# Optimization experiments

Measured on AMD Instinct MI355X. Metric: run time of the kernel, lower is better.

Reference implementation:

```python
import jax, jax.numpy as jnp
import numpy as np

N_NODES = 100000
N_EDGES = 3200000
D_IN = 128
D_OUT = 128


def setup_inputs() -> dict:
    key = jax.random.key(0)
    ks = jax.random.split(key, 7)
    x = jax.random.normal(ks[0], (N_NODES, D_IN), dtype=jnp.float32)
    weight = jax.random.normal(ks[1], (D_IN, D_OUT), dtype=jnp.float32) * (1.0 / np.sqrt(D_OUT))
    bias = jax.random.normal(ks[2], (D_OUT,), dtype=jnp.float32) * (1.0 / np.sqrt(D_OUT))
    adj_rows = jax.random.randint(ks[3], (N_EDGES,), 0, N_NODES, dtype=jnp.int32)
    adj_cols = jax.random.randint(ks[4], (N_EDGES,), 0, N_NODES, dtype=jnp.int32)
    adj_vals = jax.random.uniform(ks[5], (N_EDGES,), dtype=jnp.float32)
    # norm kept in [0.5, 1.5) to avoid division blow-up (degree-like normalizer)
    norm = jax.random.uniform(ks[6], (N_NODES, 1), dtype=jnp.float32) + 0.5
    return {"x": x, "weight": weight, "bias": bias,
            "adj_rows": adj_rows, "adj_cols": adj_cols, "adj_vals": adj_vals,
            "norm": norm}


def reference(x, weight, bias, adj_rows, adj_cols, adj_vals, norm):
    # support = input @ W               [N, D_OUT]
    support = x @ weight
    # output = spmm(adj, support): gather source rows, scale by edge value,
    # scatter-add into destination rows.
    gathered = support[adj_cols] * adj_vals[:, None]          # [E, D_OUT]
    output = jax.ops.segment_sum(gathered, adj_rows, num_segments=x.shape[0])
    output = output / norm
    return output + bias
```

## Files before the change

### kernel.cpp

```cpp
#include <hip/hip_runtime.h>

#define M_NODES 100000
#define N_EDGES 3200000
#define D 128
#define NBUCK 1563
#define FILL_CHUNK 12288
#define FILL_BLOCKS 261
#define GEMM_BLOCKS 782
#define PREP_BLOCKS (FILL_BLOCKS + GEMM_BLOCKS)
#define BUCK_CAP 4096

#define OFF_SUP16  0ull
#define OFF_BCNT   25600000ull
#define OFF_REC    25608192ull
#define WS_NEEDED  76824576ull

__device__ __forceinline__ unsigned short f2bf(float f) {
    unsigned u = __float_as_uint(f);
    u += 0x7fff + ((u >> 16) & 1);
    return (unsigned short)(u >> 16);
}
__device__ __forceinline__ float2 bfpair(unsigned u) {
    float2 r;
    r.x = __uint_as_float(u << 16);
    r.y = __uint_as_float(u & 0xffff0000u);
    return r;
}

__global__ __launch_bounds__(512) void prep_kernel(const float* __restrict__ x,
                                                   const float* __restrict__ w,
                                                   unsigned* __restrict__ sup16,
                                                   const int* __restrict__ rows,
                                                   const int* __restrict__ cols,
                                                   const float* __restrict__ vals,
                                                   int* __restrict__ bcnt,
                                                   int2* __restrict__ rec,
                                                   int M) {
    __shared__ __align__(16) char smem[37120];
    const int tid = threadIdx.x;

    if (blockIdx.x < FILL_BLOCKS) {
        int* cnt = (int*)smem;
        int* bas = (int*)(smem + 6256);
        unsigned short* lrank = (unsigned short*)(smem + 12512);
        for (int i = tid; i < NBUCK; i += 512) cnt[i] = 0;
        __syncthreads();
        const long long base = (long long)blockIdx.x * FILL_CHUNK;

#pragma unroll
        for (int i = 0; i < 6; ++i) {
            const int li = (i * 512 + tid) * 4;
            const long long e = base + li;
            if (e < N_EDGES) {
                const int4 r = *(const int4*)&rows[e];
                lrank[li + 0] = (unsigned short)atomicAdd(&cnt[r.x >> 6], 1);
                lrank[li + 1] = (unsigned short)atomicAdd(&cnt[r.y >> 6], 1);
                lrank[li + 2] = (unsigned short)atomicAdd(&cnt[r.z >> 6], 1);
                lrank[li + 3] = (unsigned short)atomicAdd(&cnt[r.w >> 6], 1);
            }
        }
        __syncthreads();
        for (int i = tid; i < NBUCK; i += 512)
            bas[i] = cnt[i] ? atomicAdd(&bcnt[i], cnt[i]) : 0;
        __syncthreads();
#pragma unroll
        for (int i = 0; i < 6; ++i) {
            const int li = (i * 512 + tid) * 4;
            const long long e = base + li;
            if (e < N_EDGES) {
                const int4   r = *(const int4*)&rows[e];
                const int4   c = *(const int4*)&cols[e];
                const float4 v = *(const float4*)&vals[e];
                int p;
                p = bas[r.x >> 6] + lrank[li + 0];
                if (p < BUCK_CAP)
                    rec[(size_t)(r.x >> 6) * BUCK_CAP + p] =
                        make_int2(c.x | ((r.x & 63) << 20), __float_as_int(v.x));
                p = bas[r.y >> 6] + lrank[li + 1];
                if (p < BUCK_CAP)
                    rec[(size_t)(r.y >> 6) * BUCK_CAP + p] =
                        make_int2(c.y | ((r.y & 63) << 20), __float_as_int(v.y));
                p = bas[r.z >> 6] + lrank[li + 2];
                if (p < BUCK_CAP)
                    rec[(size_t)(r.z >> 6) * BUCK_CAP + p] =
                        make_int2(c.z | ((r.z & 63) << 20), __float_as_int(v.z));
                p = bas[r.w >> 6] + lrank[li + 3];
                if (p < BUCK_CAP)
                    rec[(size_t)(r.w >> 6) * BUCK_CAP + p] =
                        make_int2(c.w | ((r.w & 63) << 20), __float_as_int(v.w));
            }
        }
        return;
    }

    float (*sX)[128] = (float(*)[128])smem;
    float (*sW)[128] = (float(*)[128])(smem + 16384);

    const int r0 = (blockIdx.x - FILL_BLOCKS) * 128;
    const int tx = tid & 31;
    const int ty = tid >> 5;

    float acc[8][4];
#pragma unroll
    for (int r = 0; r < 8; ++r)
#pragma unroll
        for (int c = 0; c < 4; ++c) acc[r][c] = 0.f;

    for (int c0 = 0; c0 < 128; c0 += 32) {
        {
            const int row = tid >> 3;
            const int kk  = (tid & 7) * 4;
#pragma unroll
            for (int h = 0; h < 2; ++h) {
                const int rr = row + h * 64;
                float4 v = make_float4(0.f, 0.f, 0.f, 0.f);
                if (r0 + rr < M)
                    v = *(const float4*)&x[(size_t)(r0 + rr) * D + c0 + kk];
                sX[kk + 0][rr] = v.x;
                sX[kk + 1][rr] = v.y;
                sX[kk + 2][rr] = v.z;
                sX[kk + 3][rr] = v.w;
            }
        }
#pragma unroll
        for (int i = tid; i < 1024; i += 512) {
            const int k  = i >> 5;
            const int c4 = (i & 31) * 4;
            *(float4*)&sW[k][c4] = *(const float4*)&w[(size_t)(c0 + k) * D + c4];
        }
        __syncthreads();

#pragma unroll
        for (int k = 0; k < 32; ++k) {
            const float4 wv = *(const float4*)&sW[k][tx * 4];
            const float4 xa = *(const float4*)&sX[k][ty * 8];
            const float4 xb = *(const float4*)&sX[k][ty * 8 + 4];
            const float xr[8] = {xa.x, xa.y, xa.z, xa.w, xb.x, xb.y, xb.z, xb.w};
#pragma unroll
            for (int r = 0; r < 8; ++r) {
                acc[r][0] += xr[r] * wv.x;
                acc[r][1] += xr[r] * wv.y;
                acc[r][2] += xr[r] * wv.z;
                acc[r][3] += xr[r] * wv.w;
            }
        }
        __syncthreads();
    }

#pragma unroll
    for (int r = 0; r < 8; ++r) {
        const int row = r0 + ty * 8 + r;
        if (row < M) {
            uint2 p;
            p.x = (unsigned)f2bf(acc[r][0]) | ((unsigned)f2bf(acc[r][1]) << 16);
            p.y = (unsigned)f2bf(acc[r][2]) | ((unsigned)f2bf(acc[r][3]) << 16);
            *(uint2*)&sup16[(size_t)row * 64 + tx * 2] = p;
        }
    }
}

__global__ __launch_bounds__(512) void gather_kernel(const unsigned* __restrict__ sup16,
                                                     const int* __restrict__ bcnt,
                                                     const int2* __restrict__ rec,
                                                     const float* __restrict__ norm,
                                                     const float* __restrict__ bias,
                                                     float* __restrict__ out) {
    __shared__ int2 elist[BUCK_CAP];
    __shared__ int cnt[64];
    __shared__ int rbase[65];
    const int tid = threadIdx.x;
    const int b   = blockIdx.x;

    if (tid < 64) cnt[tid] = 0;
    __syncthreads();
    const int n = min(bcnt[b], BUCK_CAP);
    const int2* __restrict__ recb = rec + (size_t)b * BUCK_CAP;

    for (int k = tid; k < n; k += 512)
        atomicAdd(&cnt[(recb[k].x >> 20) & 63], 1);
    __syncthreads();
    if (tid == 0) {
        int run = 0;
#pragma unroll
        for (int i = 0; i < 64; ++i) {
            rbase[i] = run;
            run += cnt[i];
        }
        rbase[64] = run;
    }
    __syncthreads();
    if (tid < 64) cnt[tid] = rbase[tid];
    __syncthreads();
    for (int k = tid; k < n; k += 512) {
        const int2 e = recb[k];
        const int p = atomicAdd(&cnt[(e.x >> 20) & 63], 1);
        elist[p] = make_int2(e.x & 0xFFFFF, e.y);
    }
    __syncthreads();

    const int w    = tid >> 6;
    const int lane = tid & 63;
    const unsigned* __restrict__ supl = sup16 + lane;
    const int fo = lane * 2;
    const float2 b2 = *(const float2*)&bias[fo];

#pragma unroll 1
    for (int rr = 0; rr < 8; ++rr) {
        const int rl  = w * 8 + rr;
        const int row = b * 64 + rl;
        if (row >= M_NODES) break;
        const int j0 = rbase[rl];
        const int j1 = rbase[rl + 1];
        float2 acc = make_float2(0.f, 0.f);
        int j = j0;
        for (; j + 8 <= j1; j += 8) {
            int2 e[8];
#pragma unroll
            for (int q = 0; q < 8; ++q) e[q] = elist[j + q];
            unsigned u[8];
#pragma unroll
            for (int q = 0; q < 8; ++q) u[q] = supl[(unsigned)e[q].x << 6];
#pragma unroll
            for (int q = 0; q < 8; ++q) {
                const float v = __int_as_float(e[q].y);
                const float2 p = bfpair(u[q]);
                acc.x = fmaf(p.x, v, acc.x);
                acc.y = fmaf(p.y, v, acc.y);
            }
        }
        for (; j + 2 <= j1; j += 2) {
            const int2 e0 = elist[j];
            const int2 e1 = elist[j + 1];
            const unsigned u0 = supl[(unsigned)e0.x << 6];
            const unsigned u1 = supl[(unsigned)e1.x << 6];
            const float2 p0 = bfpair(u0);
            const float2 p1 = bfpair(u1);
            const float v0 = __int_as_float(e0.y);
            const float v1 = __int_as_float(e1.y);
            acc.x = fmaf(p0.x, v0, acc.x);
            acc.y = fmaf(p0.y, v0, acc.y);
            acc.x = fmaf(p1.x, v1, acc.x);
            acc.y = fmaf(p1.y, v1, acc.y);
        }
        for (; j < j1; ++j) {
            const int2 e = elist[j];
            const unsigned u = supl[(unsigned)e.x << 6];
            const float v = __int_as_float(e.y);
            const float2 p = bfpair(u);
            acc.x = fmaf(p.x, v, acc.x);
            acc.y = fmaf(p.y, v, acc.y);
        }
        const float inv = 1.0f / norm[row];
        float2 o;
        o.x = fmaf(acc.x, inv, b2.x);
        o.y = fmaf(acc.y, inv, b2.y);
        *(float2*)&out[(size_t)row * D + fo] = o;
    }
}

__global__ __launch_bounds__(256) void gemm32_kernel(const float* __restrict__ x,
                                                     const float* __restrict__ w,
                                                     float* __restrict__ support,
                                                     int M) {
    __shared__ float sX[32][64];
    __shared__ float sW[32][128];
    const int tid = threadIdx.x;
    const int r0  = blockIdx.x * 64;
    const int tx  = tid & 31;
    const int ty  = tid >> 5;
    float acc[8][4];
#pragma unroll
    for (int r = 0; r < 8; ++r)
#pragma unroll
        for (int c = 0; c < 4; ++c) acc[r][c] = 0.f;
    for (int c0 = 0; c0 < 128; c0 += 32) {
        {
            const int row = tid >> 3;
            const int kk  = (tid & 7) * 4;
#pragma unroll
            for (int h = 0; h < 2; ++h) {
                const int rr = row + h * 32;
                float4 v = make_float4(0.f, 0.f, 0.f, 0.f);
                if (r0 + rr < M)
                    v = *(const float4*)&x[(size_t)(r0 + rr) * D + c0 + kk];
                sX[kk + 0][rr] = v.x; sX[kk + 1][rr] = v.y;
                sX[kk + 2][rr] = v.z; sX[kk + 3][rr] = v.w;
            }
        }
#pragma unroll
        for (int i = tid; i < 1024; i += 256) {
            const int k  = i >> 5;
            const int c4 = (i & 31) * 4;
            *(float4*)&sW[k][c4] = *(const float4*)&w[(size_t)(c0 + k) * D + c4];
        }
        __syncthreads();
#pragma unroll
        for (int k = 0; k < 32; ++k) {
            const float4 wv = *(const float4*)&sW[k][tx * 4];
            const float4 xa = *(const float4*)&sX[k][ty * 8];
            const float4 xb = *(const float4*)&sX[k][ty * 8 + 4];
            const float xr[8] = {xa.x, xa.y, xa.z, xa.w, xb.x, xb.y, xb.z, xb.w};
#pragma unroll
            for (int r = 0; r < 8; ++r) {
                acc[r][0] += xr[r] * wv.x; acc[r][1] += xr[r] * wv.y;
                acc[r][2] += xr[r] * wv.z; acc[r][3] += xr[r] * wv.w;
            }
        }
        __syncthreads();
    }
#pragma unroll
    for (int r = 0; r < 8; ++r) {
        const int row = r0 + ty * 8 + r;
        if (row < M)
            *(float4*)&support[(size_t)row * D + tx * 4] =
                make_float4(acc[r][0], acc[r][1], acc[r][2], acc[r][3]);
    }
}

__global__ __launch_bounds__(256) void spmm_kernel(const float* __restrict__ support,
                                                   const int* __restrict__ rows,
                                                   const int* __restrict__ cols,
                                                   const float* __restrict__ vals,
                                                   float* __restrict__ out) {
    const long long t = (long long)blockIdx.x * 256 + threadIdx.x;
    const int e = (int)(t >> 5);
    if (e >= N_EDGES) return;
    const int f   = (int)(t & 31) * 4;
    const int src = cols[e];
    const int dst = rows[e];
    const float v = vals[e];
    const float4 s = *(const float4*)&support[(size_t)src * D + f];
    float* o = &out[(size_t)dst * D + f];
    atomicAdd(o + 0, s.x * v);
    atomicAdd(o + 1, s.y * v);
    atomicAdd(o + 2, s.z * v);
    atomicAdd(o + 3, s.w * v);
}

__global__ __launch_bounds__(256) void finalize_kernel(float* __restrict__ out,
                                                       const float* __restrict__ norm,
                                                       const float* __restrict__ bias) {
    const int t = blockIdx.x * 256 + threadIdx.x;
    const int nrow = t >> 5;
    if (nrow >= M_NODES) return;
    const int f = (t & 31) * 4;
    const float inv = 1.0f / norm[nrow];
    float4 o = *(float4*)&out[(size_t)nrow * D + f];
    const float4 b = *(const float4*)&bias[f];
    o.x = o.x * inv + b.x; o.y = o.y * inv + b.y;
    o.z = o.z * inv + b.z; o.w = o.w * inv + b.w;
    *(float4*)&out[(size_t)nrow * D + f] = o;
}

extern "C" void kernel_launch(void* const* d_in, const int* in_sizes, int n_in,
                              void* d_out, int out_size, void* d_ws, size_t ws_size,
                              hipStream_t stream) {
    const float* x    = (const float*)d_in[0];
    const float* w    = (const float*)d_in[1];
    const float* bias = (const float*)d_in[2];
    const int*   rows = (const int*)d_in[3];
    const int*   cols = (const int*)d_in[4];
    const float* vals = (const float*)d_in[5];
    const float* norm = (const float*)d_in[6];
    float* out = (float*)d_out;
    char* ws = (char*)d_ws;

    if (ws_size >= WS_NEEDED) {
        unsigned* sup16 = (unsigned*)(ws + OFF_SUP16);
        int*      bcnt  = (int*)(ws + OFF_BCNT);
        int2*     rec   = (int2*)(ws + OFF_REC);

        hipMemsetAsync(bcnt, 0, NBUCK * sizeof(int), stream);
        prep_kernel<<<PREP_BLOCKS, 512, 0, stream>>>(x, w, sup16, rows, cols, vals,
                                                     bcnt, rec, M_NODES);
        gather_kernel<<<NBUCK, 512, 0, stream>>>(sup16, bcnt, rec,
                                                 norm, bias, out);
    } else {
        float* support = (float*)ws;
        gemm32_kernel<<<(M_NODES + 63) / 64, 256, 0, stream>>>(x, w, support, M_NODES);
        hipMemsetAsync(d_out, 0, (size_t)out_size * sizeof(float), stream);
        const long long spmm_threads = (long long)N_EDGES * 32;
        spmm_kernel<<<(int)((spmm_threads + 255) / 256), 256, 0, stream>>>(support, rows, cols, vals, out);
        finalize_kernel<<<(M_NODES * 32 + 255) / 256, 256, 0, stream>>>(out, norm, bias);
    }
}
```

Measured before the change: 331.3 us.

## Sort bucket edges by source-node segment to improve gather locality

The gather kernel now bins each bucket's edges by (source-node segment of 16K nodes, destination row) rather than by destination row alone, using a 512-entry block-wide prefix scan in place of the serial 64-entry scan. Each wave then walks the seven source segments in order, keeping eight row accumulators in registers. At any moment all blocks are then reading support rows from a narrower address range, which should improve L2/MALL hit rate on the random gathers. In exchange it adds scan barriers, more registers, and shorter inner loops (unroll 4 instead of 8) with more loop overhead per segment.

```diff
diff --git a/kernel.cpp b/kernel.cpp
--- a/kernel.cpp
+++ b/kernel.cpp
@@ -9,6 +9,7 @@
 #define GEMM_BLOCKS 782
 #define PREP_BLOCKS (FILL_BLOCKS + GEMM_BLOCKS)
 #define BUCK_CAP 4096
+#define NSEG 7
 
 #define OFF_SUP16  0ull
 #define OFF_BCNT   25600000ull
@@ -166,34 +167,41 @@
                                                      const float* __restrict__ bias,
                                                      float* __restrict__ out) {
     __shared__ int2 elist[BUCK_CAP];
-    __shared__ int cnt[64];
-    __shared__ int rbase[65];
+    __shared__ int cnt[512];
+    __shared__ int rbase[514];
     const int tid = threadIdx.x;
     const int b   = blockIdx.x;
 
-    if (tid < 64) cnt[tid] = 0;
+    cnt[tid] = 0;
     __syncthreads();
     const int n = min(bcnt[b], BUCK_CAP);
     const int2* __restrict__ recb = rec + (size_t)b * BUCK_CAP;
 
-    for (int k = tid; k < n; k += 512)
-        atomicAdd(&cnt[(recb[k].x >> 20) & 63], 1);
-    __syncthreads();
-    if (tid == 0) {
-        int run = 0;
-#pragma unroll
-        for (int i = 0; i < 64; ++i) {
-            rbase[i] = run;
-            run += cnt[i];
-        }
-        rbase[64] = run;
-    }
-    __syncthreads();
-    if (tid < 64) cnt[tid] = rbase[tid];
+    for (int k = tid; k < n; k += 512) {
+        const int ex = recb[k].x;
+        const int key = (((ex & 0xFFFFF) >> 14) << 6) | ((ex >> 20) & 63);
+        atomicAdd(&cnt[key], 1);
+    }
+    __syncthreads();
+    int* tsum = (int*)elist;
+    const int myc = cnt[tid];
+    tsum[tid] = myc;
+    __syncthreads();
+    for (int off = 1; off < 512; off <<= 1) {
+        const int v = (tid >= off) ? tsum[tid - off] : 0;
+        __syncthreads();
+        tsum[tid] += v;
+        __syncthreads();
+    }
+    const int excl = tsum[tid] - myc;
+    rbase[tid] = excl;
+    cnt[tid]   = excl;
+    if (tid == 0) rbase[512] = n;
     __syncthreads();
     for (int k = tid; k < n; k += 512) {
         const int2 e = recb[k];
-        const int p = atomicAdd(&cnt[(e.x >> 20) & 63], 1);
+        const int key = (((e.x & 0xFFFFF) >> 14) << 6) | ((e.x >> 20) & 63);
+        const int p = atomicAdd(&cnt[key], 1);
         elist[p] = make_int2(e.x & 0xFFFFF, e.y);
     }
     __syncthreads();
@@ -204,57 +212,55 @@
     const int fo = lane * 2;
     const float2 b2 = *(const float2*)&bias[fo];
 
+    float2 acc[8];
+#pragma unroll
+    for (int r = 0; r < 8; ++r) acc[r] = make_float2(0.f, 0.f);
+
 #pragma unroll 1
+    for (int seg = 0; seg < NSEG; ++seg) {
+        const int kbase = seg * 64 + w * 8;
+#pragma unroll
+        for (int rr = 0; rr < 8; ++rr) {
+            int j = rbase[kbase + rr];
+            const int j1 = rbase[kbase + rr + 1];
+            float2 a = acc[rr];
+            for (; j + 4 <= j1; j += 4) {
+                int2 e[4];
+#pragma unroll
+                for (int q = 0; q < 4; ++q) e[q] = elist[j + q];
+                unsigned u[4];
+#pragma unroll
+                for (int q = 0; q < 4; ++q) u[q] = supl[(unsigned)e[q].x << 6];
+#pragma unroll
+                for (int q = 0; q < 4; ++q) {
+                    const float v = __int_as_float(e[q].y);
+                    const float2 p = bfpair(u[q]);
+                    a.x = fmaf(p.x, v, a.x);
+                    a.y = fmaf(p.y, v, a.y);
+                }
+            }
+            for (; j < j1; ++j) {
+                const int2 e = elist[j];
+                const unsigned u = supl[(unsigned)e.x << 6];
+                const float v = __int_as_float(e.y);
+                const float2 p = bfpair(u);
+                a.x = fmaf(p.x, v, a.x);
+                a.y = fmaf(p.y, v, a.y);
+            }
+            acc[rr] = a;
+        }
+    }
+
+#pragma unroll
     for (int rr = 0; rr < 8; ++rr) {
-        const int rl  = w * 8 + rr;
-        const int row = b * 64 + rl;
-        if (row >= M_NODES) break;
-        const int j0 = rbase[rl];
-        const int j1 = rbase[rl + 1];
-        float2 acc = make_float2(0.f, 0.f);
-        int j = j0;
-        for (; j + 8 <= j1; j += 8) {
-            int2 e[8];
-#pragma unroll
-            for (int q = 0; q < 8; ++q) e[q] = elist[j + q];
-            unsigned u[8];
-#pragma unroll
-            for (int q = 0; q < 8; ++q) u[q] = supl[(unsigned)e[q].x << 6];
-#pragma unroll
-            for (int q = 0; q < 8; ++q) {
-                const float v = __int_as_float(e[q].y);
-                const float2 p = bfpair(u[q]);
-                acc.x = fmaf(p.x, v, acc.x);
-                acc.y = fmaf(p.y, v, acc.y);
-            }
-        }
-        for (; j + 2 <= j1; j += 2) {
-            const int2 e0 = elist[j];
-            const int2 e1 = elist[j + 1];
-            const unsigned u0 = supl[(unsigned)e0.x << 6];
-            const unsigned u1 = supl[(unsigned)e1.x << 6];
-            const float2 p0 = bfpair(u0);
-            const float2 p1 = bfpair(u1);
-            const float v0 = __int_as_float(e0.y);
-            const float v1 = __int_as_float(e1.y);
-            acc.x = fmaf(p0.x, v0, acc.x);
-            acc.y = fmaf(p0.y, v0, acc.y);
-            acc.x = fmaf(p1.x, v1, acc.x);
-            acc.y = fmaf(p1.y, v1, acc.y);
-        }
-        for (; j < j1; ++j) {
-            const int2 e = elist[j];
-            const unsigned u = supl[(unsigned)e.x << 6];
-            const float v = __int_as_float(e.y);
-            const float2 p = bfpair(u);
-            acc.x = fmaf(p.x, v, acc.x);
-            acc.y = fmaf(p.y, v, acc.y);
-        }
-        const float inv = 1.0f / norm[row];
-        float2 o;
-        o.x = fmaf(acc.x, inv, b2.x);
-        o.y = fmaf(acc.y, inv, b2.y);
-        *(float2*)&out[(size_t)row * D + fo] = o;
+        const int row = b * 64 + w * 8 + rr;
+        if (row < M_NODES) {
+            const float inv = 1.0f / norm[row];
+            float2 o;
+            o.x = fmaf(acc[rr].x, inv, b2.x);
+            o.y = fmaf(acc[rr].y, inv, b2.y);
+            *(float2*)&out[(size_t)row * D + fo] = o;
+        }
     }
 }
 
```

Result: no change. 331.6 us (+0.1%).

## Compute X@W with bf16 MFMA using split hi/lo precision emulation

Applied to the files above, without the earlier changes.

Replaces the FP32 FMA register-tiled GEMM in the prep kernel with MFMA 16x16x32 bf16 instructions. Each fp32 operand is split into high and low bf16 parts, and three MFMAs per tile approximate fp32 accuracy. The tile shrinks to 64 rows per block, so twice as many GEMM blocks are launched. The aim is to cut GEMM compute time by using the matrix cores. The cost is extra conversion work when staging into shared memory, a transposed W store that may cause bank conflicts, and cross-lane shuffles when packing the output.

```diff
diff --git a/kernel.cpp b/kernel.cpp
--- a/kernel.cpp
+++ b/kernel.cpp
@@ -6,7 +6,7 @@
 #define NBUCK 1563
 #define FILL_CHUNK 12288
 #define FILL_BLOCKS 261
-#define GEMM_BLOCKS 782
+#define GEMM_BLOCKS 1563
 #define PREP_BLOCKS (FILL_BLOCKS + GEMM_BLOCKS)
 #define BUCK_CAP 4096
 
@@ -15,10 +15,16 @@
 #define OFF_REC    25608192ull
 #define WS_NEEDED  76824576ull
 
+typedef __attribute__((ext_vector_type(8))) short short8;
+typedef __attribute__((ext_vector_type(4))) float f32x4;
+
 __device__ __forceinline__ unsigned short f2bf(float f) {
     unsigned u = __float_as_uint(f);
     u += 0x7fff + ((u >> 16) & 1);
     return (unsigned short)(u >> 16);
+}
+__device__ __forceinline__ float bf2f(unsigned short h) {
+    return __uint_as_float((unsigned)h << 16);
 }
 __device__ __forceinline__ float2 bfpair(unsigned u) {
     float2 r;
@@ -93,68 +99,86 @@
         return;
     }
 
-    float (*sX)[128] = (float(*)[128])smem;
-    float (*sW)[128] = (float(*)[128])(smem + 16384);
-
-    const int r0 = (blockIdx.x - FILL_BLOCKS) * 128;
-    const int tx = tid & 31;
-    const int ty = tid >> 5;
-
-    float acc[8][4];
-#pragma unroll
-    for (int r = 0; r < 8; ++r)
-#pragma unroll
-        for (int c = 0; c < 4; ++c) acc[r][c] = 0.f;
+    short* xh = (short*)smem;
+    short* xl = (short*)(smem + 5120);
+    short* wh = (short*)(smem + 10240);
+    short* wl = (short*)(smem + 20480);
+
+    const int r0   = (blockIdx.x - FILL_BLOCKS) * 64;
+    const int wv   = tid >> 6;
+    const int lane = tid & 63;
+    const int g    = lane >> 4;
+    const int ml   = lane & 15;
+
+    const int mt = wv & 3;
+    const int ng = (wv >> 2) * 4;
+
+    f32x4 acc[4];
+#pragma unroll
+    for (int i = 0; i < 4; ++i) acc[i] = (f32x4){0.f, 0.f, 0.f, 0.f};
 
     for (int c0 = 0; c0 < 128; c0 += 32) {
         {
-            const int row = tid >> 3;
-            const int kk  = (tid & 7) * 4;
-#pragma unroll
-            for (int h = 0; h < 2; ++h) {
-                const int rr = row + h * 64;
-                float4 v = make_float4(0.f, 0.f, 0.f, 0.f);
-                if (r0 + rr < M)
-                    v = *(const float4*)&x[(size_t)(r0 + rr) * D + c0 + kk];
-                sX[kk + 0][rr] = v.x;
-                sX[kk + 1][rr] = v.y;
-                sX[kk + 2][rr] = v.z;
-                sX[kk + 3][rr] = v.w;
-            }
-        }
-#pragma unroll
-        for (int i = tid; i < 1024; i += 512) {
-            const int k  = i >> 5;
-            const int c4 = (i & 31) * 4;
-            *(float4*)&sW[k][c4] = *(const float4*)&w[(size_t)(c0 + k) * D + c4];
-        }
-        __syncthreads();
-
-#pragma unroll
-        for (int k = 0; k < 32; ++k) {
-            const float4 wv = *(const float4*)&sW[k][tx * 4];
-            const float4 xa = *(const float4*)&sX[k][ty * 8];
-            const float4 xb = *(const float4*)&sX[k][ty * 8 + 4];
-            const float xr[8] = {xa.x, xa.y, xa.z, xa.w, xb.x, xb.y, xb.z, xb.w};
-#pragma unroll
-            for (int r = 0; r < 8; ++r) {
-                acc[r][0] += xr[r] * wv.x;
-                acc[r][1] += xr[r] * wv.y;
-                acc[r][2] += xr[r] * wv.z;
-                acc[r][3] += xr[r] * wv.w;
-            }
-        }
-        __syncthreads();
-    }
-
-#pragma unroll
-    for (int r = 0; r < 8; ++r) {
-        const int row = r0 + ty * 8 + r;
-        if (row < M) {
-            uint2 p;
-            p.x = (unsigned)f2bf(acc[r][0]) | ((unsigned)f2bf(acc[r][1]) << 16);
-            p.y = (unsigned)f2bf(acc[r][2]) | ((unsigned)f2bf(acc[r][3]) << 16);
-            *(uint2*)&sup16[(size_t)row * 64 + tx * 2] = p;
+            const int r  = tid >> 3;
+            const int k0 = (tid & 7) * 4;
+            float4 v = make_float4(0.f, 0.f, 0.f, 0.f);
+            if (r0 + r < M)
+                v = *(const float4*)&x[(size_t)(r0 + r) * D + c0 + k0];
+            unsigned short h0 = f2bf(v.x), h1 = f2bf(v.y),
+                           h2 = f2bf(v.z), h3 = f2bf(v.w);
+            unsigned short l0 = f2bf(v.x - bf2f(h0)), l1 = f2bf(v.y - bf2f(h1)),
+                           l2 = f2bf(v.z - bf2f(h2)), l3 = f2bf(v.w - bf2f(h3));
+            uint2 ph, pl;
+            ph.x = (unsigned)h0 | ((unsigned)h1 << 16);
+            ph.y = (unsigned)h2 | ((unsigned)h3 << 16);
+            pl.x = (unsigned)l0 | ((unsigned)l1 << 16);
+            pl.y = (unsigned)l2 | ((unsigned)l3 << 16);
+            *(uint2*)&xh[r * 40 + k0] = ph;
+            *(uint2*)&xl[r * 40 + k0] = pl;
+        }
+        {
+            const int k    = tid >> 4;
+            const int col0 = (tid & 15) * 8;
+            const float4 a = *(const float4*)&w[(size_t)(c0 + k) * D + col0];
+            const float4 bq = *(const float4*)&w[(size_t)(c0 + k) * D + col0 + 4];
+            const float vv[8] = {a.x, a.y, a.z, a.w, bq.x, bq.y, bq.z, bq.w};
+#pragma unroll
+            for (int j = 0; j < 8; ++j) {
+                const unsigned short h = f2bf(vv[j]);
+                wh[(col0 + j) * 40 + k] = (short)h;
+                wl[(col0 + j) * 40 + k] = (short)f2bf(vv[j] - bf2f(h));
+            }
+        }
+        __syncthreads();
+
+        const short8 a_hi = *(const short8*)&xh[(mt * 16 + ml) * 40 + g * 8];
+        const short8 a_lo = *(const short8*)&xl[(mt * 16 + ml) * 40 + g * 8];
+#pragma unroll
+        for (int i = 0; i < 4; ++i) {
+            const int col = (ng + i) * 16 + ml;
+            const short8 b_hi = *(const short8*)&wh[col * 40 + g * 8];
+            const short8 b_lo = *(const short8*)&wl[col * 40 + g * 8];
+            acc[i] = __builtin_amdgcn_mfma_f32_16x16x32_bf16(a_hi, b_hi, acc[i], 0, 0, 0);
+            acc[i] = __builtin_amdgcn_mfma_f32_16x16x32_bf16(a_lo, b_hi, acc[i], 0, 0, 0);
+            acc[i] = __builtin_amdgcn_mfma_f32_16x16x32_bf16(a_hi, b_lo, acc[i], 0, 0, 0);
+        }
+        __syncthreads();
+    }
+
+#pragma unroll
+    for (int i = 0; i < 4; ++i) {
+#pragma unroll
+        for (int reg = 0; reg < 4; ++reg) {
+            const float mine  = acc[i][reg];
+            const float other = __shfl_xor(mine, 1);
+            if (!(lane & 1)) {
+                const unsigned uo = (unsigned)f2bf(mine) | ((unsigned)f2bf(other) << 16);
+                const int grow = r0 + mt * 16 + g * 4 + reg;
+                if (grow < M) {
+                    const int word = (wv >> 2) * 32 + i * 8 + (ml >> 1);
+                    sup16[(size_t)grow * 64 + word] = uo;
+                }
+            }
         }
     }
 }
```

Result: faster. 317.4 us, median of 2 (-4.2%).
